# Kernel optimization log

Hardware: AMD Instinct MI355X
Metric: run time of the kernel (lower is better)

Reference implementation:

```python
import jax, jax.numpy as jnp
import numpy as np

ACT_BITS = 8
GROUP = 64
EPS = 1e-8


def absmax_quantize_dequant(x, bits=ACT_BITS, group_size=GROUP):
    """Group-wise (per-token) absmax fake-quantize to signed `bits` ints, then dequantize.
    Straight-through estimator: gradient flows as identity through the quantizer."""
    qmax = 2 ** (bits - 1) - 1  # 127 for 8 bits
    orig_shape = x.shape
    xg = x.reshape(*orig_shape[:-1], orig_shape[-1] // group_size, group_size)
    scale = jnp.maximum(jnp.max(jnp.abs(xg), axis=-1, keepdims=True), EPS)
    q = jnp.clip(jnp.round(xg / scale * qmax), -qmax, qmax)
    xq = (q * scale / qmax).reshape(orig_shape)
    # STE: forward = xq, backward = identity
    return x + jax.lax.stop_gradient(xq - x)


def binary_weight_quantize_centered(W):
    """Per-row centered binarization: sign(W - mean) scaled by per-row mean |.| (BitNet 1-bit).
    Straight-through estimator on the weights."""
    Wc = W - jnp.mean(W, axis=1, keepdims=True)          # [out, in]
    alpha = jnp.mean(jnp.abs(Wc), axis=1, keepdims=True)  # per-row scale [out, 1]
    Wb = jnp.sign(Wc) * alpha
    return W + jax.lax.stop_gradient(Wb - W)


def setup_inputs() -> dict:
    key = jax.random.key(0)
    kx, kw = jax.random.split(key)
    B, S, D_IN, D_OUT = 4, 2048, 4096, 4096
    x = jax.random.normal(kx, (B, S, D_IN), dtype=jnp.float32)
    # kaiming-uniform-ish init scale
    bound = float(np.sqrt(1.0 / D_IN))
    W = jax.random.uniform(kw, (D_OUT, D_IN), dtype=jnp.float32, minval=-bound, maxval=bound)
    return {"x": x, "W": W}


def reference(x, W):
    x_q = absmax_quantize_dequant(x)
    Wb = binary_weight_quantize_centered(W)
    # F.linear(x_q, Wb): y[b,s,o] = sum_d x_q[b,s,d] * Wb[o,d]
    return jnp.einsum('bsd,od->bso', x_q, Wb)
```

## Files before the change

### kernel.cpp

```cpp
#include <hip/hip_runtime.h>
#include <hip/hip_bf16.h>
#include <stdint.h>
#include <stddef.h>

typedef _Float16 f16;
typedef _Float16 f16x4 __attribute__((ext_vector_type(4)));
typedef _Float16 f16x8 __attribute__((ext_vector_type(8)));
typedef float    f32x4 __attribute__((ext_vector_type(4)));

__device__ __forceinline__ void gload16(const void* g, void* l) {
  __builtin_amdgcn_global_load_lds(
      (__attribute__((address_space(1))) void*)g,
      (__attribute__((address_space(3))) void*)l,
      16, 0, 0);
}

__global__ __launch_bounds__(256) void prep_w_kernel(
    const float* __restrict__ W, f16* __restrict__ sgn,
    float* __restrict__ alpha, int K)
{
  const int row = blockIdx.x;
  const int tid = threadIdx.x;
  const float4* Wr = (const float4*)(W + (size_t)row * K);

  float4 v[4];
#pragma unroll
  for (int j = 0; j < 4; ++j) v[j] = Wr[j * 256 + tid];

  __shared__ float red1[4];
  __shared__ float red2[4];

  float s = 0.f;
#pragma unroll
  for (int j = 0; j < 4; ++j) s += (v[j].x + v[j].y) + (v[j].z + v[j].w);
#pragma unroll
  for (int m = 32; m >= 1; m >>= 1) s += __shfl_xor(s, m);
  if ((tid & 63) == 0) red1[tid >> 6] = s;
  __syncthreads();
  const float mean = (red1[0] + red1[1] + red1[2] + red1[3]) * (1.0f / 4096.0f);

  float a = 0.f;
#pragma unroll
  for (int j = 0; j < 4; ++j) {
    a += fabsf(v[j].x - mean) + fabsf(v[j].y - mean) +
         fabsf(v[j].z - mean) + fabsf(v[j].w - mean);
  }
#pragma unroll
  for (int m = 32; m >= 1; m >>= 1) a += __shfl_xor(a, m);
  if ((tid & 63) == 0) red2[tid >> 6] = a;

  f16x4* so = (f16x4*)(sgn + (size_t)row * K);
#pragma unroll
  for (int j = 0; j < 4; ++j) {
    float w0 = v[j].x - mean, w1 = v[j].y - mean,
          w2 = v[j].z - mean, w3 = v[j].w - mean;
    f16x4 o;
    o[0] = (f16)((w0 > 0.f) ? 1.f : ((w0 < 0.f) ? -1.f : 0.f));
    o[1] = (f16)((w1 > 0.f) ? 1.f : ((w1 < 0.f) ? -1.f : 0.f));
    o[2] = (f16)((w2 > 0.f) ? 1.f : ((w2 < 0.f) ? -1.f : 0.f));
    o[3] = (f16)((w3 > 0.f) ? 1.f : ((w3 < 0.f) ? -1.f : 0.f));
    so[j * 256 + tid] = o;
  }
  __syncthreads();
  if (tid == 0)
    alpha[row] = (red2[0] + red2[1] + red2[2] + red2[3]) * (1.0f / 4096.0f);
}

__global__ __launch_bounds__(256) void quant_x_kernel(
    const float4* __restrict__ x4, f16x4* __restrict__ xq4)
{
  const int i = blockIdx.x * 256 + threadIdx.x;
  float4 v = x4[i];
  float am = fmaxf(fmaxf(fabsf(v.x), fabsf(v.y)),
                   fmaxf(fabsf(v.z), fabsf(v.w)));
  am = fmaxf(am, __shfl_xor(am, 1));
  am = fmaxf(am, __shfl_xor(am, 2));
  am = fmaxf(am, __shfl_xor(am, 4));
  am = fmaxf(am, __shfl_xor(am, 8));
  const float scale = fmaxf(am, 1e-8f);

  float q0 = fminf(fmaxf(rintf(v.x / scale * 127.0f), -127.0f), 127.0f);
  float q1 = fminf(fmaxf(rintf(v.y / scale * 127.0f), -127.0f), 127.0f);
  float q2 = fminf(fmaxf(rintf(v.z / scale * 127.0f), -127.0f), 127.0f);
  float q3 = fminf(fmaxf(rintf(v.w / scale * 127.0f), -127.0f), 127.0f);

  f16x4 o;
  o[0] = (f16)(q0 * scale / 127.0f);
  o[1] = (f16)(q1 * scale / 127.0f);
  o[2] = (f16)(q2 * scale / 127.0f);
  o[3] = (f16)(q3 * scale / 127.0f);
  xq4[i] = o;
}

#define BM 128
#define BN 128
#define BK 32

__global__ __launch_bounds__(256) void gemm_kernel(
    const f16* __restrict__ A,
    const f16* __restrict__ Bt,
    const float* __restrict__ alpha,
    float* __restrict__ C, int M, int N, int K)
{
  __shared__ __align__(16) f16 As[BM * BK];
  __shared__ __align__(16) f16 Bs[BN * BK];

  const int tid  = threadIdx.x;
  const int wave = tid >> 6;
  const int lane = tid & 63;
  const int bm = blockIdx.y * BM;
  const int bn = blockIdx.x * BN;
  const int wr = (wave >> 1) * 64;
  const int wc = (wave & 1) * 64;

  const int srow = tid >> 2;
  const int scol = (tid & 3) * 8;
  const f16* Ag0 = A  + (size_t)(bm + srow) * K + scol;
  const f16* Ag1 = A  + (size_t)(bm + 64 + srow) * K + scol;
  const f16* Bg0 = Bt + (size_t)(bn + srow) * K + scol;
  const f16* Bg1 = Bt + (size_t)(bn + 64 + srow) * K + scol;

  char* lA0 = (char*)As + wave * 1024;
  char* lA1 = (char*)As + 4096 + wave * 1024;
  char* lB0 = (char*)Bs + wave * 1024;
  char* lB1 = (char*)Bs + 4096 + wave * 1024;

  const int lrow = lane & 15;
  const int lko  = (lane >> 4) * 8;

  f32x4 acc[4][4] = {};

  const int nk = K / BK;
  for (int kt = 0; kt < nk; ++kt) {
    const int ko = kt * BK;
    gload16(Ag0 + ko, lA0);
    gload16(Ag1 + ko, lA1);
    gload16(Bg0 + ko, lB0);
    gload16(Bg1 + ko, lB1);
    __syncthreads();

    f16x8 af[4], bf[4];
#pragma unroll
    for (int mi = 0; mi < 4; ++mi)
      af[mi] = *(const f16x8*)&As[(wr + mi * 16 + lrow) * BK + lko];
#pragma unroll
    for (int ni = 0; ni < 4; ++ni)
      bf[ni] = *(const f16x8*)&Bs[(wc + ni * 16 + lrow) * BK + lko];

#pragma unroll
    for (int mi = 0; mi < 4; ++mi)
#pragma unroll
      for (int ni = 0; ni < 4; ++ni)
        acc[mi][ni] = __builtin_amdgcn_mfma_f32_16x16x32_f16(
            af[mi], bf[ni], acc[mi][ni], 0, 0, 0);
    __syncthreads();
  }

  const int crow = bm + wr + ((lane >> 4) << 2);
  const int ccol = bn + wc + (lane & 15);
#pragma unroll
  for (int ni = 0; ni < 4; ++ni) {
    const int n = ccol + ni * 16;
    const float al = alpha[n];
#pragma unroll
    for (int mi = 0; mi < 4; ++mi) {
#pragma unroll
      for (int r = 0; r < 4; ++r) {
        C[(size_t)(crow + mi * 16 + r) * N + n] = acc[mi][ni][r] * al;
      }
    }
  }
}

extern "C" void kernel_launch(void* const* d_in, const int* in_sizes, int n_in,
                              void* d_out, int out_size, void* d_ws, size_t ws_size,
                              hipStream_t stream) {
  const float* x = (const float*)d_in[0];
  const float* W = (const float*)d_in[1];
  float* y = (float*)d_out;

  const int K = 4096;
  const int M = in_sizes[0] / K;
  const int N = in_sizes[1] / K;

  f16*   xq    = (f16*)d_ws;
  f16*   sgn   = (f16*)((char*)d_ws + (size_t)M * K * 2);
  float* alpha = (float*)((char*)d_ws + (size_t)M * K * 2 + (size_t)N * K * 2);

  prep_w_kernel<<<N, 256, 0, stream>>>(W, sgn, alpha, K);

  const int n4 = (M * K) / 4;
  quant_x_kernel<<<n4 / 256, 256, 0, stream>>>((const float4*)x, (f16x4*)xq);

  dim3 grid(N / BN, M / BM);
  gemm_kernel<<<grid, 256, 0, stream>>>(xq, sgn, alpha, y, M, N, K);
}
```

Baseline: 577.0 us.

## Rewrite GEMM as 256x256 double-buffered pipelined kernel with swizzled LDS

Replaces the simple 128x128x32 GEMM, which synchronised twice per K step, with a 256x256x64 tile run by 512 threads. It double-buffers 128KB of LDS and interleaves global-to-LDS loads with MFMA quarters under barriers and s_setprio. An XOR swizzle on the LDS layout avoids bank conflicts, and a blockIdx remap groups tiles for L2 locality. The aim is to hide memory latency and raise MFMA utilisation. The cost is heavy register pressure and 128KB of LDS per block, which limits occupancy, plus complex wraparound prefetch logic.

```diff
diff --git a/kernel.cpp b/kernel.cpp
--- a/kernel.cpp
+++ b/kernel.cpp
@@ -13,6 +13,12 @@
       (__attribute__((address_space(1))) void*)g,
       (__attribute__((address_space(3))) void*)l,
       16, 0, 0);
+}
+
+__device__ __forceinline__ void BAR() {
+  asm volatile("" ::: "memory");
+  __builtin_amdgcn_s_barrier();
+  asm volatile("" ::: "memory");
 }
 
 __global__ __launch_bounds__(256) void prep_w_kernel(
@@ -92,81 +98,175 @@
   xq4[i] = o;
 }
 
-#define BM 128
-#define BN 128
-#define BK 32
-
-__global__ __launch_bounds__(256) void gemm_kernel(
+#define BM 256
+#define BN 256
+#define BK 64
+
+__global__ __launch_bounds__(512, 2) void gemm_kernel(
     const f16* __restrict__ A,
     const f16* __restrict__ Bt,
     const float* __restrict__ alpha,
     float* __restrict__ C, int M, int N, int K)
 {
-  __shared__ __align__(16) f16 As[BM * BK];
-  __shared__ __align__(16) f16 Bs[BN * BK];
+  __shared__ __align__(16) char smem[131072];
 
   const int tid  = threadIdx.x;
   const int wave = tid >> 6;
   const int lane = tid & 63;
-  const int bm = blockIdx.y * BM;
-  const int bn = blockIdx.x * BN;
-  const int wr = (wave >> 1) * 64;
-  const int wc = (wave & 1) * 64;
-
-  const int srow = tid >> 2;
-  const int scol = (tid & 3) * 8;
-  const f16* Ag0 = A  + (size_t)(bm + srow) * K + scol;
-  const f16* Ag1 = A  + (size_t)(bm + 64 + srow) * K + scol;
-  const f16* Bg0 = Bt + (size_t)(bn + srow) * K + scol;
-  const f16* Bg1 = Bt + (size_t)(bn + 64 + srow) * K + scol;
-
-  char* lA0 = (char*)As + wave * 1024;
-  char* lA1 = (char*)As + 4096 + wave * 1024;
-  char* lB0 = (char*)Bs + wave * 1024;
-  char* lB1 = (char*)Bs + 4096 + wave * 1024;
+  const int wm = wave >> 2;
+  const int wn = wave & 3;
+
+  const int nbx = N / BN;
+  const int nwg = gridDim.x;
+  const int cpx = nwg >> 3;
+  const int bid = blockIdx.x;
+  const int swz = (bid & 7) * cpx + (bid >> 3);
+  const int bn = (swz % nbx) * BN;
+  const int bm = (swz / nbx) * BM;
 
   const int lrow = lane & 15;
-  const int lko  = (lane >> 4) * 8;
-
-  f32x4 acc[4][4] = {};
+  const int lk   = (lane >> 4) * 8;
+  const int kxr  = (lane & 4) ? 16 : 0;
+  const int lko2 = (lk ^ kxr) * 2;
+  const int aob  = wm * 16384 + lrow * 128 + lko2;
+  const int bob  = 32768 + (wn >> 1) * 16384 + ((wn & 1) * 64 + lrow) * 128 + lko2;
+
+  const int srow = lane >> 3;
+  const int ksrc = ((lane & 7) * 8) ^ ((srow & 4) ? 16 : 0);
+  const size_t lsoff = (size_t)srow * K + ksrc;
+
+#define RDA(BUF, mi, kh) (*(const f16x8*)(smem + (BUF) + aob + (mi)*2048 + (kh)*64))
+#define RDB(BUF, ni, kh) (*(const f16x8*)(smem + (BUF) + bob + (ni)*2048 + (kh)*64))
+
+#define STAGE(LDSOFF, MAT, GROW, T) do {                                        \
+    const f16* _s = (MAT) + (size_t)((GROW) + wave * 8) * K + (size_t)(T) * 64; \
+    gload16(_s + lsoff, smem + (LDSOFF) + wave * 1024);                         \
+    gload16(_s + (size_t)64 * K + lsoff, smem + (LDSOFF) + 8192 + wave * 1024); \
+  } while (0)
+
+#define MMQ(AARR, BARR, MBASE) do {                                             \
+    _Pragma("unroll")                                                           \
+    for (int mi = 0; mi < 4; ++mi) {                                            \
+      _Pragma("unroll")                                                         \
+      for (int ni = 0; ni < 4; ++ni) {                                          \
+        acc[(MBASE) + mi][ni] = __builtin_amdgcn_mfma_f32_16x16x32_f16(         \
+            AARR[(MBASE) + mi], BARR[ni], acc[(MBASE) + mi][ni], 0, 0, 0);      \
+      }                                                                         \
+    }                                                                           \
+  } while (0)
+
+  f32x4 acc[8][4] = {};
+  f16x8 a0[8], a1[8], bq0[4], bq1[4];
 
   const int nk = K / BK;
-  for (int kt = 0; kt < nk; ++kt) {
-    const int ko = kt * BK;
-    gload16(Ag0 + ko, lA0);
-    gload16(Ag1 + ko, lA1);
-    gload16(Bg0 + ko, lB0);
-    gload16(Bg1 + ko, lB1);
-    __syncthreads();
-
-    f16x8 af[4], bf[4];
-#pragma unroll
-    for (int mi = 0; mi < 4; ++mi)
-      af[mi] = *(const f16x8*)&As[(wr + mi * 16 + lrow) * BK + lko];
-#pragma unroll
-    for (int ni = 0; ni < 4; ++ni)
-      bf[ni] = *(const f16x8*)&Bs[(wc + ni * 16 + lrow) * BK + lko];
-
-#pragma unroll
-    for (int mi = 0; mi < 4; ++mi)
-#pragma unroll
-      for (int ni = 0; ni < 4; ++ni)
-        acc[mi][ni] = __builtin_amdgcn_mfma_f32_16x16x32_f16(
-            af[mi], bf[ni], acc[mi][ni], 0, 0, 0);
-    __syncthreads();
-  }
-
-  const int crow = bm + wr + ((lane >> 4) << 2);
-  const int ccol = bn + wc + (lane & 15);
+
+  STAGE(0,             A,  bm,       0);
+  STAGE(16384,         A,  bm + 128, 0);
+  STAGE(32768,         Bt, bn,       0);
+  STAGE(49152,         Bt, bn + 128, 0);
+  STAGE(65536 + 32768, Bt, bn,       1);
+  asm volatile("s_waitcnt vmcnt(2)" ::: "memory");
+  BAR();
+
+  for (int it = 0; it < nk / 2; ++it) {
+    const int t1 = 2 * it + 1;
+    int t2 = 2 * it + 2; if (t2 >= nk) t2 -= nk;
+    int t3 = 2 * it + 3; if (t3 >= nk) t3 -= nk;
+
+#pragma unroll
+    for (int mi = 0; mi < 4; ++mi) a0[mi] = RDA(0, mi, 0);
+#pragma unroll
+    for (int ni = 0; ni < 4; ++ni) bq0[ni] = RDB(0, ni, 0);
+#pragma unroll
+    for (int mi = 4; mi < 8; ++mi) a0[mi] = RDA(0, mi, 0);
+    STAGE(65536 + 49152, Bt, bn + 128, t1);
+    BAR();
+    __builtin_amdgcn_s_setprio(1);
+    MMQ(a0, bq0, 0);
+    __builtin_amdgcn_s_setprio(0);
+    BAR();
+
+#pragma unroll
+    for (int mi = 0; mi < 4; ++mi) a1[mi] = RDA(0, mi, 1);
+#pragma unroll
+    for (int ni = 0; ni < 4; ++ni) bq1[ni] = RDB(0, ni, 1);
+    STAGE(65536, A, bm, t1);
+    BAR();
+    __builtin_amdgcn_s_setprio(1);
+    MMQ(a0, bq0, 4);
+    __builtin_amdgcn_s_setprio(0);
+    BAR();
+
+#pragma unroll
+    for (int mi = 4; mi < 8; ++mi) a1[mi] = RDA(0, mi, 1);
+    STAGE(65536 + 16384, A, bm + 128, t1);
+    BAR();
+    __builtin_amdgcn_s_setprio(1);
+    MMQ(a1, bq1, 0);
+    __builtin_amdgcn_s_setprio(0);
+    BAR();
+
+    STAGE(32768, Bt, bn, t2);
+    asm volatile("s_waitcnt vmcnt(2)" ::: "memory");
+    BAR();
+    __builtin_amdgcn_s_setprio(1);
+    MMQ(a1, bq1, 4);
+    __builtin_amdgcn_s_setprio(0);
+    BAR();
+
+#pragma unroll
+    for (int mi = 0; mi < 4; ++mi) a0[mi] = RDA(65536, mi, 0);
+#pragma unroll
+    for (int ni = 0; ni < 4; ++ni) bq0[ni] = RDB(65536, ni, 0);
+#pragma unroll
+    for (int mi = 4; mi < 8; ++mi) a0[mi] = RDA(65536, mi, 0);
+    STAGE(49152, Bt, bn + 128, t2);
+    BAR();
+    __builtin_amdgcn_s_setprio(1);
+    MMQ(a0, bq0, 0);
+    __builtin_amdgcn_s_setprio(0);
+    BAR();
+
+#pragma unroll
+    for (int mi = 0; mi < 4; ++mi) a1[mi] = RDA(65536, mi, 1);
+#pragma unroll
+    for (int ni = 0; ni < 4; ++ni) bq1[ni] = RDB(65536, ni, 1);
+    STAGE(0, A, bm, t2);
+    BAR();
+    __builtin_amdgcn_s_setprio(1);
+    MMQ(a0, bq0, 4);
+    __builtin_amdgcn_s_setprio(0);
+    BAR();
+
+#pragma unroll
+    for (int mi = 4; mi < 8; ++mi) a1[mi] = RDA(65536, mi, 1);
+    STAGE(16384, A, bm + 128, t2);
+    BAR();
+    __builtin_amdgcn_s_setprio(1);
+    MMQ(a1, bq1, 0);
+    __builtin_amdgcn_s_setprio(0);
+    BAR();
+
+    STAGE(65536 + 32768, Bt, bn, t3);
+    asm volatile("s_waitcnt vmcnt(2)" ::: "memory");
+    BAR();
+    __builtin_amdgcn_s_setprio(1);
+    MMQ(a1, bq1, 4);
+    __builtin_amdgcn_s_setprio(0);
+    BAR();
+  }
+
+  const int r0 = bm + wm * 128 + ((lane >> 4) << 2);
+  const int c0 = bn + wn * 64 + (lane & 15);
 #pragma unroll
   for (int ni = 0; ni < 4; ++ni) {
-    const int n = ccol + ni * 16;
-    const float al = alpha[n];
-#pragma unroll
-    for (int mi = 0; mi < 4; ++mi) {
+    const int n = c0 + ni * 16;
+    const float alv = alpha[n];
+#pragma unroll
+    for (int mi = 0; mi < 8; ++mi) {
 #pragma unroll
       for (int r = 0; r < 4; ++r) {
-        C[(size_t)(crow + mi * 16 + r) * N + n] = acc[mi][ni][r] * al;
+        C[(size_t)(r0 + mi * 16 + r) * N + n] = acc[mi][ni][r] * alv;
       }
     }
   }
@@ -192,6 +292,6 @@
   const int n4 = (M * K) / 4;
   quant_x_kernel<<<n4 / 256, 256, 0, stream>>>((const float4*)x, (f16x4*)xq);
 
-  dim3 grid(N / BN, M / BM);
-  gemm_kernel<<<grid, 256, 0, stream>>>(xq, sgn, alpha, y, M, N, K);
-}
+  const int nblk = (M / BM) * (N / BN);
+  gemm_kernel<<<nblk, 512, 0, stream>>>(xq, sgn, alpha, y, M, N, K);
+}
```

Measured after the change: 505.9 us. 12.3% less time.
